# Performance work log

Measured on AMD Instinct MI355X. Metric: run time of the kernel, lower is better.

The kernel has to match this reference:

```python
import jax, jax.numpy as jnp
import numpy as np

H = 512                      # hidden_size
CUTOFFS = [20000, 50000, 100000]
PF = 4                       # project_factor
N, T = 2, 1024               # batch, seq_len
NUM_TAILS = len(CUTOFFS) - 1


def setup_inputs() -> dict:
    key = jax.random.key(0)
    ks = jax.random.split(key, 6)
    x = jax.random.normal(ks[0], (N, T, H), dtype=jnp.float32)
    scale = 0.02
    # head_weight: [H, cutoffs[0] + num_tails] (head tokens + one logit per tail cluster)
    head_weight = jax.random.normal(ks[1], (H, CUTOFFS[0] + NUM_TAILS), dtype=jnp.float32) * scale
    # tail 0: proj size H // pf = 128, tail size 30000
    p0 = max(1, H // PF)
    tail_proj_0 = jax.random.normal(ks[2], (H, p0), dtype=jnp.float32) * scale
    tail_w_0 = jax.random.normal(ks[3], (p0, CUTOFFS[1] - CUTOFFS[0]), dtype=jnp.float32) * scale
    # tail 1: proj size H // pf^2 = 32, tail size 50000
    p1 = max(1, H // PF ** 2)
    tail_proj_1 = jax.random.normal(ks[4], (H, p1), dtype=jnp.float32) * scale
    tail_w_1 = jax.random.normal(ks[5], (p1, CUTOFFS[2] - CUTOFFS[1]), dtype=jnp.float32) * scale
    return {
        "x": x,
        "head_weight": head_weight,
        "tail_proj_0": tail_proj_0,
        "tail_w_0": tail_w_0,
        "tail_proj_1": tail_proj_1,
        "tail_w_1": tail_w_1,
    }


def reference(x, head_weight, tail_proj_0, tail_w_0, tail_proj_1, tail_w_1):
    """Adaptive softmax ('softmax' mode): per-token distribution over vocab.

    x: [N, T, H] -> out: [N, T, V] where V = CUTOFFS[-1].
    """
    # head logits over [head tokens + tail-cluster logits]
    head_logits = jnp.einsum("nth,hv->ntv", x, head_weight)   # [N,T,c0+num_tails]
    head_sm = jax.nn.softmax(head_logits, axis=-1)
    parts = [head_sm[..., : CUTOFFS[0]]]
    tails = ((tail_proj_0, tail_w_0), (tail_proj_1, tail_w_1))
    for i, (proj, w) in enumerate(tails):
        # low-rank projection then tail vocab logits
        tail_logits = jnp.einsum("ntp,pv->ntv", jnp.einsum("nth,hp->ntp", x, proj), w)
        tail_sm = jax.nn.softmax(tail_logits, axis=-1)
        cluster_prob = head_sm[..., CUTOFFS[0] + i : CUTOFFS[0] + i + 1]  # [N,T,1]
        parts.append(tail_sm * cluster_prob)
    return jnp.concatenate(parts, axis=-1)  # [N,T,V]
```

## Files before the change

kernel.cpp:

```cpp
#include <hip/hip_runtime.h>
#include <cstdint>
#include <cstddef>

typedef unsigned short u16;
typedef short bf16x8 __attribute__((ext_vector_type(8)));
typedef float f32x4 __attribute__((ext_vector_type(4)));

__device__ __forceinline__ u16 f2bf(float f) {
  unsigned u = __float_as_uint(f);
  u += 0x7fffu + ((u >> 16) & 1u);
  return (u16)(u >> 16);
}

__global__ __launch_bounds__(256) void proj_kernel(const float* __restrict__ x,
                                                   const float* __restrict__ tp0,
                                                   const float* __restrict__ tp1,
                                                   u16* __restrict__ xb,
                                                   u16* __restrict__ p0,
                                                   u16* __restrict__ p1) {
  __shared__ float xr[512];
  const int t = blockIdx.x;
  const int j = threadIdx.x;
  {
    float2 v = ((const float2*)(x + (size_t)t * 512))[j];
    xr[2 * j] = v.x;
    xr[2 * j + 1] = v.y;
    ushort2 o;
    o.x = f2bf(v.x);
    o.y = f2bf(v.y);
    ((ushort2*)(xb + (size_t)t * 512))[j] = o;
  }
  __syncthreads();
  if (j < 128) {
    float a = 0.f;
    for (int h = 0; h < 512; ++h) a += xr[h] * tp0[h * 128 + j];
    p0[t * 128 + j] = f2bf(a);
  } else if (j < 160) {
    const int j2 = j - 128;
    float a = 0.f;
    for (int h = 0; h < 512; ++h) a += xr[h] * tp1[h * 32 + j2];
    p1[t * 32 + j2] = f2bf(a);
  }
}

__global__ __launch_bounds__(256) void transpose_cast_kernel(const float* __restrict__ W,
                                                             u16* __restrict__ Wt,
                                                             int K, int V, int Vpad) {
  __shared__ float tile[64][65];
  const int v0 = blockIdx.x * 64, k0 = blockIdx.y * 64;
  for (int l = threadIdx.x; l < 4096; l += 256) {
    int kl = l >> 6, vl = l & 63;
    int kg = k0 + kl, vg = v0 + vl;
    tile[kl][vl] = (kg < K && vg < V) ? W[(size_t)kg * V + vg] : 0.f;
  }
  __syncthreads();
  for (int l = threadIdx.x; l < 4096; l += 256) {
    int vl = l >> 6, kl = l & 63;
    int vg = v0 + vl, kg = k0 + kl;
    if (vg < Vpad && kg < K) Wt[(size_t)vg * K + kg] = f2bf(tile[kl][vl]);
  }
}

__global__ __launch_bounds__(256) void zero_kernel(float* __restrict__ p, int n) {
  int i = blockIdx.x * 256 + threadIdx.x;
  if (i < n) p[i] = 0.f;
}

template <int K, int MODE>
__global__ __launch_bounds__(256) void gemm_pass(const u16* __restrict__ A,
                                                 const u16* __restrict__ Wt,
                                                 float* __restrict__ out,
                                                 float* __restrict__ clus,
                                                 float* __restrict__ sums,
                                                 const float* __restrict__ fac,
                                                 int V, int outColOff, int secIdx) {
  constexpr int LDT = 40;
  __shared__ __align__(16) u16 As[128 * LDT];
  __shared__ __align__(16) u16 Bs[128 * LDT];
  const int tid = threadIdx.x;
  const int lane = tid & 63, wave = tid >> 6;
  const int t0 = blockIdx.y * 128;
  const int v0 = blockIdx.x * 128;

  f32x4 acc[2][8];
#pragma unroll
  for (int i = 0; i < 2; ++i)
#pragma unroll
    for (int j = 0; j < 8; ++j) acc[i][j] = (f32x4){0.f, 0.f, 0.f, 0.f};

  const int rl = lane & 15;
  const int kb = (lane >> 4) * 8;

  for (int kk = 0; kk < K; kk += 32) {
#pragma unroll
    for (int c0 = 0; c0 < 2; ++c0) {
      int c = c0 * 256 + tid;
      int r = c >> 2, kc = c & 3;
      *(uint4*)&As[r * LDT + kc * 8] =
          *(const uint4*)&A[(size_t)(t0 + r) * K + kk + kc * 8];
      *(uint4*)&Bs[r * LDT + kc * 8] =
          *(const uint4*)&Wt[(size_t)(v0 + r) * K + kk + kc * 8];
    }
    __syncthreads();

    bf16x8 fa[2], fb[8];
#pragma unroll
    for (int rf = 0; rf < 2; ++rf)
      fa[rf] = *(const bf16x8*)&As[(wave * 32 + rf * 16 + rl) * LDT + kb];
#pragma unroll
    for (int cf = 0; cf < 8; ++cf)
      fb[cf] = *(const bf16x8*)&Bs[(cf * 16 + rl) * LDT + kb];
#pragma unroll
    for (int rf = 0; rf < 2; ++rf)
#pragma unroll
      for (int cf = 0; cf < 8; ++cf)
        acc[rf][cf] =
            __builtin_amdgcn_mfma_f32_16x16x32_bf16(fa[rf], fb[cf], acc[rf][cf], 0, 0, 0);
    __syncthreads();
  }

  const int rbase = (lane >> 4) * 4;

  if (MODE <= 1) {
#pragma unroll
    for (int rf = 0; rf < 2; ++rf) {
#pragma unroll
      for (int r = 0; r < 4; ++r) {
        const int tok = t0 + wave * 32 + rf * 16 + rbase + r;
        float s = 0.f;
#pragma unroll
        for (int cf = 0; cf < 8; ++cf) {
          const int colv = v0 + cf * 16 + rl;
          const float l = acc[rf][cf][r];
          const float e = __expf(l);
          s += (colv < V) ? e : 0.f;
          if (MODE == 0) {
            if (colv >= 20000 && colv < V) clus[tok * 2 + (colv - 20000)] = l;
          }
        }
#pragma unroll
        for (int m = 1; m < 16; m <<= 1) s += __shfl_xor(s, m, 64);
        if (rl == 0) atomicAdd(&sums[tok * 3 + secIdx], s);
      }
    }
  } else {
    const int lim = (MODE == 2) ? 20000 : V;
#pragma unroll
    for (int rf = 0; rf < 2; ++rf) {
#pragma unroll
      for (int r = 0; r < 4; ++r) {
        const int tok = t0 + wave * 32 + rf * 16 + rbase + r;
        const float f = fac[tok * 3 + secIdx];
        float* orow = out + (size_t)tok * 100000 + outColOff + v0;
#pragma unroll
        for (int cf = 0; cf < 8; ++cf) {
          const int colv = v0 + cf * 16 + rl;
          if (colv < lim)
            __builtin_nontemporal_store(__expf(acc[rf][cf][r]) * f,
                                        orow + cf * 16 + rl);
        }
      }
    }
  }
}

__global__ void factors_kernel(const float* __restrict__ sums,
                               const float* __restrict__ clus,
                               float* __restrict__ fac) {
  int t = blockIdx.x * blockDim.x + threadIdx.x;
  if (t >= 2048) return;
  float inv_sh = 1.f / sums[t * 3 + 0];
  fac[t * 3 + 0] = inv_sh;
  float cp0 = __expf(clus[t * 2 + 0]) * inv_sh;
  float cp1 = __expf(clus[t * 2 + 1]) * inv_sh;
  fac[t * 3 + 1] = cp0 / sums[t * 3 + 1];
  fac[t * 3 + 2] = cp1 / sums[t * 3 + 2];
}

extern "C" void kernel_launch(void* const* d_in, const int* in_sizes, int n_in,
                              void* d_out, int out_size, void* d_ws, size_t ws_size,
                              hipStream_t stream) {
  const float* x   = (const float*)d_in[0];
  const float* hw  = (const float*)d_in[1];
  const float* tp0 = (const float*)d_in[2];
  const float* tw0 = (const float*)d_in[3];
  const float* tp1 = (const float*)d_in[4];
  const float* tw1 = (const float*)d_in[5];
  float* out = (float*)d_out;
  char* ws = (char*)d_ws;

  u16* wt_h    = (u16*)(ws + 0);
  u16* wt_t0   = (u16*)(ws + 20578304);
  u16* wt_t1   = (u16*)(ws + 28278784);
  u16* x_bf    = (u16*)(ws + 31481856);
  u16* p0_bf   = (u16*)(ws + 33579008);
  u16* p1_bf   = (u16*)(ws + 34103296);
  float* clus  = (float*)(ws + 34234368);
  float* sums  = (float*)(ws + 34250752);
  float* fac   = (float*)(ws + 34275328);

  zero_kernel<<<24, 256, 0, stream>>>(sums, 2048 * 3);
  proj_kernel<<<2048, 256, 0, stream>>>(x, tp0, tp1, x_bf, p0_bf, p1_bf);
  transpose_cast_kernel<<<dim3(314, 8), 256, 0, stream>>>(hw,  wt_h,  512, 20002, 20096);
  transpose_cast_kernel<<<dim3(470, 2), 256, 0, stream>>>(tw0, wt_t0, 128, 30000, 30080);
  transpose_cast_kernel<<<dim3(782, 1), 256, 0, stream>>>(tw1, wt_t1, 32,  50000, 50048);

  gemm_pass<512, 0><<<dim3(157, 16), 256, 0, stream>>>(x_bf,  wt_h,  nullptr, clus, sums, nullptr, 20002, 0, 0);
  gemm_pass<128, 1><<<dim3(235, 16), 256, 0, stream>>>(p0_bf, wt_t0, nullptr, nullptr, sums, nullptr, 30000, 0, 1);
  gemm_pass<32,  1><<<dim3(391, 16), 256, 0, stream>>>(p1_bf, wt_t1, nullptr, nullptr, sums, nullptr, 50000, 0, 2);

  factors_kernel<<<8, 256, 0, stream>>>(sums, clus, fac);

  gemm_pass<512, 2><<<dim3(157, 16), 256, 0, stream>>>(x_bf,  wt_h,  out, nullptr, nullptr, fac, 20002, 0, 0);
  gemm_pass<128, 3><<<dim3(235, 16), 256, 0, stream>>>(p0_bf, wt_t0, out, nullptr, nullptr, fac, 30000, 20000, 1);
  gemm_pass<32,  3><<<dim3(391, 16), 256, 0, stream>>>(p1_bf, wt_t1, out, nullptr, nullptr, fac, 50000, 50000, 2);
}
```

Before: 1.453 ms.

## Use direct global-to-LDS loads in GEMM and skip LDS for K=32 tail

The GEMM mainloop now stages A and B tiles with global_load_lds (direct global-to-LDS DMA) into unpadded 32-wide LDS rows instead of register round-trips into padded rows. A new LDS-free kernel serves the K=32 tail, loading MFMA fragments straight from global memory. The epilogue is factored into a shared helper, and the output stores become plain stores instead of nontemporal ones. Removing the padding may introduce LDS bank conflicts on fragment reads, and dropping nontemporal stores could increase cache pollution from the large output writes.

Result: no change. 1.435 ms (-1.3%).

```diff
diff --git a/kernel.cpp b/kernel.cpp
--- a/kernel.cpp
+++ b/kernel.cpp
@@ -10,6 +10,12 @@
   unsigned u = __float_as_uint(f);
   u += 0x7fffu + ((u >> 16) & 1u);
   return (u16)(u >> 16);
+}
+
+__device__ __forceinline__ void gload_lds16(const u16* g, u16* l) {
+  __builtin_amdgcn_global_load_lds(
+      (const __attribute__((address_space(1))) void*)g,
+      (__attribute__((address_space(3))) void*)l, 16, 0, 0);
 }
 
 __global__ __launch_bounds__(256) void proj_kernel(const float* __restrict__ x,
@@ -66,6 +72,55 @@
   if (i < n) p[i] = 0.f;
 }
 
+template <int MODE>
+__device__ __forceinline__ void epilogue(f32x4 (&acc)[2][8], int lane, int wave,
+                                         int t0, int v0, float* __restrict__ out,
+                                         float* __restrict__ clus,
+                                         float* __restrict__ sums,
+                                         const float* __restrict__ fac,
+                                         int V, int outColOff, int secIdx) {
+  const int rl = lane & 15;
+  const int rbase = (lane >> 4) * 4;
+  if (MODE <= 1) {
+#pragma unroll
+    for (int rf = 0; rf < 2; ++rf) {
+#pragma unroll
+      for (int r = 0; r < 4; ++r) {
+        const int tok = t0 + wave * 32 + rf * 16 + rbase + r;
+        float s = 0.f;
+#pragma unroll
+        for (int cf = 0; cf < 8; ++cf) {
+          const int colv = v0 + cf * 16 + rl;
+          const float l = acc[rf][cf][r];
+          s += (colv < V) ? __expf(l) : 0.f;
+          if (MODE == 0) {
+            if (colv >= 20000 && colv < V) clus[tok * 2 + (colv - 20000)] = l;
+          }
+        }
+#pragma unroll
+        for (int m = 1; m < 16; m <<= 1) s += __shfl_xor(s, m, 64);
+        if (rl == 0) atomicAdd(&sums[tok * 3 + secIdx], s);
+      }
+    }
+  } else {
+    const int lim = (MODE == 2) ? 20000 : V;
+#pragma unroll
+    for (int rf = 0; rf < 2; ++rf) {
+#pragma unroll
+      for (int r = 0; r < 4; ++r) {
+        const int tok = t0 + wave * 32 + rf * 16 + rbase + r;
+        const float f = fac[tok * 3 + secIdx];
+        float* orow = out + (size_t)tok * 100000 + outColOff + v0;
+#pragma unroll
+        for (int cf = 0; cf < 8; ++cf) {
+          const int colv = v0 + cf * 16 + rl;
+          if (colv < lim) orow[cf * 16 + rl] = __expf(acc[rf][cf][r]) * f;
+        }
+      }
+    }
+  }
+}
+
 template <int K, int MODE>
 __global__ __launch_bounds__(256) void gemm_pass(const u16* __restrict__ A,
                                                  const u16* __restrict__ Wt,
@@ -74,9 +129,8 @@
                                                  float* __restrict__ sums,
                                                  const float* __restrict__ fac,
                                                  int V, int outColOff, int secIdx) {
-  constexpr int LDT = 40;
-  __shared__ __align__(16) u16 As[128 * LDT];
-  __shared__ __align__(16) u16 Bs[128 * LDT];
+  __shared__ __align__(16) u16 As[128 * 32];
+  __shared__ __align__(16) u16 Bs[128 * 32];
   const int tid = threadIdx.x;
   const int lane = tid & 63, wave = tid >> 6;
   const int t0 = blockIdx.y * 128;
@@ -91,25 +145,26 @@
   const int rl = lane & 15;
   const int kb = (lane >> 4) * 8;
 
+  const int crow = lane >> 2;
+  const int ccol = (lane & 3) * 8;
+
   for (int kk = 0; kk < K; kk += 32) {
 #pragma unroll
-    for (int c0 = 0; c0 < 2; ++c0) {
-      int c = c0 * 256 + tid;
-      int r = c >> 2, kc = c & 3;
-      *(uint4*)&As[r * LDT + kc * 8] =
-          *(const uint4*)&A[(size_t)(t0 + r) * K + kk + kc * 8];
-      *(uint4*)&Bs[r * LDT + kc * 8] =
-          *(const uint4*)&Wt[(size_t)(v0 + r) * K + kk + kc * 8];
+    for (int i = 0; i < 2; ++i) {
+      const int c = wave * 2 + i;
+      const int row = c * 16 + crow;
+      gload_lds16(&A[(size_t)(t0 + row) * K + kk + ccol], &As[c * 512]);
+      gload_lds16(&Wt[(size_t)(v0 + row) * K + kk + ccol], &Bs[c * 512]);
     }
     __syncthreads();
 
     bf16x8 fa[2], fb[8];
 #pragma unroll
     for (int rf = 0; rf < 2; ++rf)
-      fa[rf] = *(const bf16x8*)&As[(wave * 32 + rf * 16 + rl) * LDT + kb];
+      fa[rf] = *(const bf16x8*)&As[(wave * 32 + rf * 16 + rl) * 32 + kb];
 #pragma unroll
     for (int cf = 0; cf < 8; ++cf)
-      fb[cf] = *(const bf16x8*)&Bs[(cf * 16 + rl) * LDT + kb];
+      fb[cf] = *(const bf16x8*)&Bs[(cf * 16 + rl) * 32 + kb];
 #pragma unroll
     for (int rf = 0; rf < 2; ++rf)
 #pragma unroll
@@ -119,49 +174,45 @@
     __syncthreads();
   }
 
-  const int rbase = (lane >> 4) * 4;
-
-  if (MODE <= 1) {
-#pragma unroll
-    for (int rf = 0; rf < 2; ++rf) {
-#pragma unroll
-      for (int r = 0; r < 4; ++r) {
-        const int tok = t0 + wave * 32 + rf * 16 + rbase + r;
-        float s = 0.f;
-#pragma unroll
-        for (int cf = 0; cf < 8; ++cf) {
-          const int colv = v0 + cf * 16 + rl;
-          const float l = acc[rf][cf][r];
-          const float e = __expf(l);
-          s += (colv < V) ? e : 0.f;
-          if (MODE == 0) {
-            if (colv >= 20000 && colv < V) clus[tok * 2 + (colv - 20000)] = l;
-          }
-        }
-#pragma unroll
-        for (int m = 1; m < 16; m <<= 1) s += __shfl_xor(s, m, 64);
-        if (rl == 0) atomicAdd(&sums[tok * 3 + secIdx], s);
-      }
-    }
-  } else {
-    const int lim = (MODE == 2) ? 20000 : V;
-#pragma unroll
-    for (int rf = 0; rf < 2; ++rf) {
-#pragma unroll
-      for (int r = 0; r < 4; ++r) {
-        const int tok = t0 + wave * 32 + rf * 16 + rbase + r;
-        const float f = fac[tok * 3 + secIdx];
-        float* orow = out + (size_t)tok * 100000 + outColOff + v0;
-#pragma unroll
-        for (int cf = 0; cf < 8; ++cf) {
-          const int colv = v0 + cf * 16 + rl;
-          if (colv < lim)
-            __builtin_nontemporal_store(__expf(acc[rf][cf][r]) * f,
-                                        orow + cf * 16 + rl);
-        }
-      }
-    }
-  }
+  epilogue<MODE>(acc, lane, wave, t0, v0, out, clus, sums, fac, V, outColOff, secIdx);
+}
+
+template <int MODE>
+__global__ __launch_bounds__(256) void gemm_tiny(const u16* __restrict__ A,
+                                                 const u16* __restrict__ Wt,
+                                                 float* __restrict__ out,
+                                                 float* __restrict__ clus,
+                                                 float* __restrict__ sums,
+                                                 const float* __restrict__ fac,
+                                                 int V, int outColOff, int secIdx) {
+  const int tid = threadIdx.x;
+  const int lane = tid & 63, wave = tid >> 6;
+  const int t0 = blockIdx.y * 128;
+  const int v0 = blockIdx.x * 128;
+  const int rl = lane & 15;
+  const int kb = (lane >> 4) * 8;
+
+  f32x4 acc[2][8];
+#pragma unroll
+  for (int i = 0; i < 2; ++i)
+#pragma unroll
+    for (int j = 0; j < 8; ++j) acc[i][j] = (f32x4){0.f, 0.f, 0.f, 0.f};
+
+  bf16x8 fa[2], fb[8];
+#pragma unroll
+  for (int rf = 0; rf < 2; ++rf)
+    fa[rf] = *(const bf16x8*)&A[(size_t)(t0 + wave * 32 + rf * 16 + rl) * 32 + kb];
+#pragma unroll
+  for (int cf = 0; cf < 8; ++cf)
+    fb[cf] = *(const bf16x8*)&Wt[(size_t)(v0 + cf * 16 + rl) * 32 + kb];
+#pragma unroll
+  for (int rf = 0; rf < 2; ++rf)
+#pragma unroll
+    for (int cf = 0; cf < 8; ++cf)
+      acc[rf][cf] =
+          __builtin_amdgcn_mfma_f32_16x16x32_bf16(fa[rf], fb[cf], acc[rf][cf], 0, 0, 0);
+
+  epilogue<MODE>(acc, lane, wave, t0, v0, out, clus, sums, fac, V, outColOff, secIdx);
 }
 
 __global__ void factors_kernel(const float* __restrict__ sums,
@@ -207,11 +258,11 @@
 
   gemm_pass<512, 0><<<dim3(157, 16), 256, 0, stream>>>(x_bf,  wt_h,  nullptr, clus, sums, nullptr, 20002, 0, 0);
   gemm_pass<128, 1><<<dim3(235, 16), 256, 0, stream>>>(p0_bf, wt_t0, nullptr, nullptr, sums, nullptr, 30000, 0, 1);
-  gemm_pass<32,  1><<<dim3(391, 16), 256, 0, stream>>>(p1_bf, wt_t1, nullptr, nullptr, sums, nullptr, 50000, 0, 2);
+  gemm_tiny<1><<<dim3(391, 16), 256, 0, stream>>>(p1_bf, wt_t1, nullptr, nullptr, sums, nullptr, 50000, 0, 2);
 
   factors_kernel<<<8, 256, 0, stream>>>(sums, clus, fac);
 
   gemm_pass<512, 2><<<dim3(157, 16), 256, 0, stream>>>(x_bf,  wt_h,  out, nullptr, nullptr, fac, 20002, 0, 0);
   gemm_pass<128, 3><<<dim3(235, 16), 256, 0, stream>>>(p0_bf, wt_t0, out, nullptr, nullptr, fac, 30000, 20000, 1);
-  gemm_pass<32,  3><<<dim3(391, 16), 256, 0, stream>>>(p1_bf, wt_t1, out, nullptr, nullptr, fac, 50000, 50000, 2);
-}
+  gemm_tiny<3><<<dim3(391, 16), 256, 0, stream>>>(p1_bf, wt_t1, out, nullptr, nullptr, fac, 50000, 50000, 2);
+}
```
